# Kernel tuning notes

Measured on AMD Instinct MI355X. Metric: run time of the kernel, lower is better.

## Reference

```python
import jax, jax.numpy as jnp
import numpy as np

EPS = 1e-5

def layernorm(x, g, b):
    mu = x.mean(-1, keepdims=True)
    var = ((x - mu) ** 2).mean(-1, keepdims=True)
    return (x - mu) / jnp.sqrt(var + EPS) * g + b

def segment_softmax(logits, seg, num_seg):
    # logits: [E, H, Q]; softmax over edges sharing the same target segment
    m = jax.ops.segment_max(logits, seg, num_segments=num_seg)
    ex = jnp.exp(logits - m[seg])
    s = jax.ops.segment_sum(ex, seg, num_segments=num_seg)
    return ex / s[seg]

def mha(x, Kw, Qw, Vw, tgt, src, n_tgt):
    # x: [N_src, C]; Kw/Vw: [H, C, D]; Qw: [H, Q, D]
    xK = jnp.einsum('nc,hcd->hnd', x, Kw)
    alpha = jnp.einsum('hqd,hnd->hqn', Qw, xK)            # [H, Q, N_src]
    a_e = alpha.transpose(2, 0, 1)[src]                   # [E, H, Q] per-edge logits
    w = segment_softmax(a_e, tgt, n_tgt)                  # sparse softmax over sources per target
    xV = jnp.einsum('nc,hcd->hnd', x, Vw)                 # [H, N_src, D]
    msg = w[..., None] * xV.transpose(1, 0, 2)[src][:, :, None, :]  # [E, H, Q, D]
    return jax.ops.segment_sum(msg, tgt, num_segments=n_tgt)        # [n_tgt, H, Q, D]

def block(x, tgt, src, n_tgt, Kw, Qw, Vw, g0, b0, W1, W2, g1, b1):
    Qn = Qw.shape[1]
    h = mha(x, Kw, Qw, Vw, tgt, src, n_tgt) + Qw          # [n_tgt, H, Q, D]
    h = h.transpose(0, 2, 1, 3).reshape(n_tgt, Qn, -1)    # [n_tgt, Q, hidden]
    h = layernorm(h, g0, b0)
    m = jax.nn.relu(jax.nn.relu(h @ W1) @ W2)             # MLP(Linear,ReLU,Linear) + outer ReLU
    h = layernorm(h + m, g1, b1)
    return h.sum(axis=1)                                  # [n_tgt, hidden]

def setup_inputs() -> dict:
    key = jax.random.key(0)
    ks = jax.random.split(key, 12)
    N, M, E, C, H, Q, D = 50000, 20000, 1000000, 128, 4, 1, 32
    HID = H * D
    s = 0.1
    inp = {
        'x_0': jax.random.normal(ks[0], (N, C), jnp.float32),
        'node_idx': jax.random.randint(ks[1], (E,), 0, N),
        'hedge_idx': jax.random.randint(ks[2], (E,), 0, M),
        'n_nodes': N,
        'n_hedges': M,
        'v2e_K': jax.random.normal(ks[3], (H, C, D), jnp.float32) * s,
        'v2e_Q': jax.random.normal(ks[4], (H, Q, D), jnp.float32) * s,
        'v2e_V': jax.random.normal(ks[5], (H, C, D), jnp.float32) * s,
        'v2e_ln0_g': jnp.ones((HID,), jnp.float32),
        'v2e_ln0_b': jnp.zeros((HID,), jnp.float32),
        'v2e_W1': jax.random.normal(ks[6], (HID, HID), jnp.float32) * s,
        'v2e_W2': jax.random.normal(ks[7], (HID, HID), jnp.float32) * s,
        'v2e_ln1_g': jnp.ones((HID,), jnp.float32),
        'v2e_ln1_b': jnp.zeros((HID,), jnp.float32),
        'e2v_K': jax.random.normal(ks[8], (H, HID, D), jnp.float32) * s,
        'e2v_Q': jax.random.normal(ks[9], (H, Q, D), jnp.float32) * s,
        'e2v_V': jax.random.normal(ks[10], (H, HID, D), jnp.float32) * s,
        'e2v_ln0_g': jnp.ones((HID,), jnp.float32),
        'e2v_ln0_b': jnp.zeros((HID,), jnp.float32),
        'e2v_W1': jax.random.normal(ks[11], (HID, HID), jnp.float32) * s,
        'e2v_W2': jax.random.normal(jax.random.fold_in(key, 99), (HID, HID), jnp.float32) * s,
        'e2v_ln1_g': jnp.ones((HID,), jnp.float32),
        'e2v_ln1_b': jnp.zeros((HID,), jnp.float32),
    }
    return inp

def reference(x_0, node_idx, hedge_idx, n_nodes, n_hedges,
              v2e_K, v2e_Q, v2e_V, v2e_ln0_g, v2e_ln0_b, v2e_W1, v2e_W2, v2e_ln1_g, v2e_ln1_b,
              e2v_K, e2v_Q, e2v_V, e2v_ln0_g, e2v_ln0_b, e2v_W1, e2v_W2, e2v_ln1_g, e2v_ln1_b):
    # vertex -> hyperedge: neighborhood = incidence^T, targets = hyperedges, sources = nodes
    x_1 = jax.nn.relu(block(x_0, hedge_idx, node_idx, n_hedges,
                            v2e_K, v2e_Q, v2e_V, v2e_ln0_g, v2e_ln0_b,
                            v2e_W1, v2e_W2, v2e_ln1_g, v2e_ln1_b))
    # hyperedge -> vertex: neighborhood = incidence, targets = nodes, sources = hyperedges
    x_0_out = jax.nn.relu(block(x_1, node_idx, hedge_idx, n_nodes,
                                e2v_K, e2v_Q, e2v_V, e2v_ln0_g, e2v_ln0_b,
                                e2v_W1, e2v_W2, e2v_ln1_g, e2v_ln1_b))
    return x_0_out, x_1
```

## Files before the change

kernel.cpp:

```cpp
#include <hip/hip_runtime.h>
#include <math.h>

typedef __attribute__((ext_vector_type(8))) short bf16x8;
typedef __attribute__((ext_vector_type(4))) float f32x4;

#define CSR_P 256

__device__ __forceinline__ unsigned short f2bf(float f){
  union { float f; unsigned int u; } c; c.f = f;
  unsigned int u = c.u;
  u += 0x7fff + ((u >> 16) & 1);
  return (unsigned short)(u >> 16);
}

__device__ __forceinline__ float wsum64(float v){
  #pragma unroll
  for (int off = 32; off > 0; off >>= 1) v += __shfl_xor(v, off, 64);
  return v;
}

__global__ __launch_bounds__(256) void prep2_kernel(
    const float* __restrict__ K0, const float* __restrict__ Q0, const float* __restrict__ V0,
    const float* __restrict__ W10, const float* __restrict__ W20,
    const float* __restrict__ K1, const float* __restrict__ Q1, const float* __restrict__ V1,
    const float* __restrict__ W11, const float* __restrict__ W21,
    float* __restrict__ kq0, unsigned short* __restrict__ btV0,
    unsigned short* __restrict__ btW10, unsigned short* __restrict__ btW20,
    float* __restrict__ kq1, unsigned short* __restrict__ btV1,
    unsigned short* __restrict__ btW11, unsigned short* __restrict__ btW21){
  const float *K, *Q, *V, *W1, *W2; float* kq;
  unsigned short *btV, *btW1, *btW2;
  if (blockIdx.y == 0){ K=K0; Q=Q0; V=V0; W1=W10; W2=W20; kq=kq0; btV=btV0; btW1=btW10; btW2=btW20; }
  else                { K=K1; Q=Q1; V=V1; W1=W11; W2=W21; kq=kq1; btV=btV1; btW1=btW11; btW2=btW21; }
  int i = blockIdx.x * 256 + threadIdx.x;
  if (i < 512){
    int h = i >> 7, c = i & 127;
    const float* Kp = K + (size_t)h * 4096 + (size_t)c * 32;
    const float* Qp = Q + h * 32;
    float s = 0.f;
    #pragma unroll
    for (int d = 0; d < 32; ++d) s += Kp[d] * Qp[d];
    kq[i] = s;
    return;
  }
  int j = i - 512;
  if (j < 16384){
    int n = j >> 7, k = j & 127;
    int h = n >> 5, d = n & 31;
    btV[j] = f2bf(V[(size_t)h * 4096 + (size_t)k * 32 + d]);
    return;
  }
  j -= 16384;
  if (j < 16384){
    int n = j >> 7, k = j & 127;
    btW1[j] = f2bf(W1[(size_t)k * 128 + n]);
    return;
  }
  j -= 16384;
  if (j < 16384){
    int n = j >> 7, k = j & 127;
    btW2[j] = f2bf(W2[(size_t)k * 128 + n]);
  }
}

__global__ __launch_bounds__(256) void logits_kernel(const float* __restrict__ x,
                                                     const float* __restrict__ kq,
                                                     float* __restrict__ expl,
                                                     unsigned short* __restrict__ xb,
                                                     unsigned short* __restrict__ xv,
                                                     int R){
  int row = (blockIdx.x << 2) + (threadIdx.x >> 6);
  if (row > R) return;
  int lane = threadIdx.x & 63;
  if (row == R){
    if (lane < 4) expl[4 * (size_t)R + lane] = 0.f;
    ((unsigned*)xv)[((size_t)R << 6) + lane] = 0u;
    return;
  }
  float x1 = x[128 * (size_t)row + lane];
  float x2 = x[128 * (size_t)row + lane + 64];
  xb[128 * (size_t)row + lane]      = f2bf(x1);
  xb[128 * (size_t)row + lane + 64] = f2bf(x2);
  float p0 = x1 * kq[lane]       + x2 * kq[lane + 64];
  float p1 = x1 * kq[128 + lane] + x2 * kq[192 + lane];
  float p2 = x1 * kq[256 + lane] + x2 * kq[320 + lane];
  float p3 = x1 * kq[384 + lane] + x2 * kq[448 + lane];
  p0 = wsum64(p0); p1 = wsum64(p1); p2 = wsum64(p2); p3 = wsum64(p3);
  if (lane == 0)
    *(float4*)(expl + 4 * (size_t)row) =
        make_float4(__expf(p0), __expf(p1), __expf(p2), __expf(p3));
}

__global__ __launch_bounds__(256) void hist2_kernel(const int* __restrict__ tgt0, int NB0,
                                                    const int* __restrict__ tgt1, int NB1,
                                                    int E,
                                                    int* __restrict__ counts0,
                                                    int* __restrict__ counts1){
  const int* tgt; int NB; int* counts;
  if (blockIdx.y == 0){ tgt = tgt0; NB = NB0; counts = counts0; }
  else                { tgt = tgt1; NB = NB1; counts = counts1; }
  __shared__ int hist[256];
  for (int i = threadIdx.x; i < NB; i += 256) hist[i] = 0;
  __syncthreads();
  int chunk = (E + CSR_P - 1) / CSR_P;
  int b0 = blockIdx.x * chunk, b1 = min(b0 + chunk, E);
  for (int e = b0 + threadIdx.x; e < b1; e += 256)
    atomicAdd(&hist[tgt[e] >> 8], 1);
  __syncthreads();
  for (int i = threadIdx.x; i < NB; i += 256)
    counts[i * CSR_P + blockIdx.x] = hist[i];
}

__global__ __launch_bounds__(256) void bscan_kernel(const int* __restrict__ counts0, int NB0,
                                                    const int* __restrict__ counts1,
                                                    int* __restrict__ blkoff0, int* __restrict__ blkoff1,
                                                    int* __restrict__ btot0, int* __restrict__ btot1){
  int i = blockIdx.x;
  const int* counts; int* blkoff; int* btot; int b;
  if (i < NB0){ counts = counts0; blkoff = blkoff0; btot = btot0; b = i; }
  else        { counts = counts1; blkoff = blkoff1; btot = btot1; b = i - NB0; }
  __shared__ int wtmp[5];
  int tid = threadIdx.x, lane = tid & 63, wv = tid >> 6;
  int c = counts[b * CSR_P + tid];
  int s = c;
  #pragma unroll
  for (int off = 1; off < 64; off <<= 1){
    int t = __shfl_up(s, off, 64);
    if (lane >= off) s += t;
  }
  if (lane == 63) wtmp[wv] = s;
  __syncthreads();
  if (tid == 0){
    int a0 = wtmp[0], a1 = wtmp[1], a2 = wtmp[2], a3 = wtmp[3];
    wtmp[0] = 0; wtmp[1] = a0; wtmp[2] = a0 + a1; wtmp[3] = a0 + a1 + a2;
    wtmp[4] = a0 + a1 + a2 + a3;
  }
  __syncthreads();
  blkoff[b * CSR_P + tid] = s - c + wtmp[wv];
  if (tid == 0) btot[b] = wtmp[4];
}

__global__ __launch_bounds__(64) void base_scan_kernel(const int* __restrict__ btot0, int NB0,
                                                       int* __restrict__ base0,
                                                       const int* __restrict__ btot1, int NB1,
                                                       int* __restrict__ base1){
  int lane = threadIdx.x;
  for (int pass = 0; pass < 2; ++pass){
    const int* bt = pass ? btot1 : btot0;
    int* bs       = pass ? base1 : base0;
    int NB        = pass ? NB1   : NB0;
    int carry = 0;
    for (int s0 = 0; s0 < NB; s0 += 64){
      int i = s0 + lane;
      int v = (i < NB) ? bt[i] : 0;
      int s = v;
      #pragma unroll
      for (int off = 1; off < 64; off <<= 1){
        int t = __shfl_up(s, off, 64);
        if (lane >= off) s += t;
      }
      if (i < NB) bs[i] = carry + s - v;
      carry += __shfl(s, 63, 64);
    }
  }
}

__global__ __launch_bounds__(256) void scatter2_kernel(
    const int* __restrict__ tgt0, const int* __restrict__ src0, int NB0,
    const int* __restrict__ base0, const int* __restrict__ blkoff0, int2* __restrict__ pairs0,
    const int* __restrict__ tgt1, const int* __restrict__ src1, int NB1,
    const int* __restrict__ base1, const int* __restrict__ blkoff1, int2* __restrict__ pairs1,
    int E){
  const int *tgt, *src, *bbase, *boff; int NB; int2* pairs;
  if (blockIdx.y == 0){ tgt=tgt0; src=src0; bbase=base0; boff=blkoff0; NB=NB0; pairs=pairs0; }
  else                { tgt=tgt1; src=src1; bbase=base1; boff=blkoff1; NB=NB1; pairs=pairs1; }
  __shared__ int cur[256];
  for (int i = threadIdx.x; i < NB; i += 256)
    cur[i] = bbase[i] + boff[i * CSR_P + blockIdx.x];
  __syncthreads();
  int chunk = (E + CSR_P - 1) / CSR_P;
  int b0 = blockIdx.x * chunk, b1 = min(b0 + chunk, E);
  for (int e = b0 + threadIdx.x; e < b1; e += 256){
    int t = tgt[e];
    int pos = atomicAdd(&cur[t >> 8], 1);
    pairs[pos] = make_int2(src[e], t);
  }
}

__global__ __launch_bounds__(1024) void build2_kernel(
    const int* __restrict__ base0, const int* __restrict__ btot0, int NB0,
    const int2* __restrict__ pairs0, int n0, int d0,
    int* __restrict__ rp0, int* __restrict__ kc0, int* __restrict__ col0,
    const int* __restrict__ base1, const int* __restrict__ btot1, int NB1,
    const int2* __restrict__ pairs1, int n1, int d1,
    int* __restrict__ rp1, int* __restrict__ kc1, int* __restrict__ col1){
  int b = blockIdx.x;
  const int *bbase, *bt; const int2* pairs; int n_tgt, dummy;
  int *rowptr, *kcnt, *col;
  if (blockIdx.y == 0){
    if (b >= NB0) return;
    bbase=base0; bt=btot0; pairs=pairs0; n_tgt=n0; dummy=d0; rowptr=rp0; kcnt=kc0; col=col0;
  } else {
    if (b >= NB1) return;
    bbase=base1; bt=btot1; pairs=pairs1; n_tgt=n1; dummy=d1; rowptr=rp1; kcnt=kc1; col=col1;
  }
  __shared__ int hist[256];
  __shared__ int excl[256];
  __shared__ int cur[256];
  int tid = threadIdx.x;
  int start = bbase[b];
  int end   = start + bt[b];
  int col_base = ((start + 3) & ~3) + (b << 10);
  for (int i = tid; i < 256; i += 1024) hist[i] = 0;
  __syncthreads();
  for (int e = start + tid; e < end; e += 1024)
    atomicAdd(&hist[pairs[e].y & 255], 1);
  __syncthreads();
  if (tid < 64){
    int lane = tid;
    int p0 = (hist[4 * lane]     + 3) & ~3;
    int p1 = (hist[4 * lane + 1] + 3) & ~3;
    int p2 = (hist[4 * lane + 2] + 3) & ~3;
    int p3 = (hist[4 * lane + 3] + 3) & ~3;
    int tsum = p0 + p1 + p2 + p3;
    int s = tsum;
    #pragma unroll
    for (int off = 1; off < 64; off <<= 1){
      int t = __shfl_up(s, off, 64);
      if (lane >= off) s += t;
    }
    int e0 = s - tsum;
    excl[4 * lane]     = e0;
    excl[4 * lane + 1] = e0 + p0;
    excl[4 * lane + 2] = e0 + p0 + p1;
    excl[4 * lane + 3] = e0 + p0 + p1 + p2;
  }
  __syncthreads();
  int t0 = b << 8;
  int valid = min(256, n_tgt - t0);
  for (int i = tid; i < valid; i += 1024){
    rowptr[t0 + i] = col_base + excl[i];
    kcnt[t0 + i]   = (hist[i] + 3) & ~3;
  }
  for (int i = tid; i < 256; i += 1024) cur[i] = excl[i];
  __syncthreads();
  for (int e = start + tid; e < end; e += 1024){
    int2 p = pairs[e];
    int pos = atomicAdd(&cur[p.y & 255], 1);
    col[col_base + pos] = p.x;
  }
  __syncthreads();
  for (int i = tid; i < valid; i += 1024){
    int hc = hist[i], pc = (hc + 3) & ~3;
    int base = col_base + excl[i];
    for (int j = hc; j < pc; ++j) col[base + j] = dummy;
  }
}

__global__ __launch_bounds__(256) void agg_kernel(const int* __restrict__ rowptr,
                                                  const int* __restrict__ kcnt,
                                                  const int* __restrict__ col,
                                                  const float* __restrict__ expl,
                                                  const unsigned short* __restrict__ xV,
                                                  const float* __restrict__ qvec,
                                                  const float* __restrict__ g0,
                                                  const float* __restrict__ b0,
                                                  float* __restrict__ h_out,
                                                  unsigned short* __restrict__ hb_out,
                                                  int n_tgt){
  int wid = (blockIdx.x << 2) + (threadIdx.x >> 6);
  if (wid >= n_tgt) return;
  int lane = threadIdx.x & 63;
  unsigned head = (unsigned)(lane >> 4);
  int beg = rowptr[wid];
  int k   = kcnt[wid];

  const unsigned* xv32 = (const unsigned*)xV;
  float accx = 0.f, accy = 0.f, sumw = 0.f;
  #pragma unroll 2
  for (int e = 0; e < k; e += 4){
    int4 cc = *(const int4*)(col + beg + e);
    #pragma unroll
    for (int q = 0; q < 4; ++q){
      int se = (q == 0) ? cc.x : (q == 1) ? cc.y : (q == 2) ? cc.z : cc.w;
      float a = expl[((unsigned)se << 2) + head];
      unsigned v = xv32[((unsigned)se << 6) + lane];
      union { unsigned u; float f; } lo, hi;
      lo.u = v << 16;
      hi.u = v & 0xffff0000u;
      sumw += a;
      accx += a * lo.f;
      accy += a * hi.f;
    }
  }
  float inv = (sumw > 0.f) ? 1.f / sumw : 0.f;
  accx *= inv; accy *= inv;

  float2 q2 = *(const float2*)(qvec + 2 * lane);
  accx += q2.x; accy += q2.y;

  float mean = wsum64(accx + accy) * (1.f / 128.f);
  float dx = accx - mean, dy = accy - mean;
  float var = wsum64(dx * dx + dy * dy) * (1.f / 128.f);
  float rstd = rsqrtf(var + 1e-5f);
  float2 g = *(const float2*)(g0 + 2 * lane);
  float2 b = *(const float2*)(b0 + 2 * lane);
  float ox = dx * rstd * g.x + b.x;
  float oy = dy * rstd * g.y + b.y;
  *(float2*)(h_out + 128 * (size_t)wid + 2 * lane) = make_float2(ox, oy);
  unsigned int pk = ((unsigned int)f2bf(oy) << 16) | (unsigned int)f2bf(ox);
  *(unsigned int*)(hb_out + 128 * (size_t)wid + 2 * lane) = pk;
}

__global__ __launch_bounds__(256) void gemm_xv(const unsigned short* __restrict__ A,
                                               const unsigned short* __restrict__ Bt,
                                               unsigned short* __restrict__ C, int R){
  __shared__ unsigned short As[64 * 136];
  __shared__ unsigned short Bs[128 * 136];
  int tid = threadIdx.x;
  int row0 = blockIdx.x * 64;

  #pragma unroll
  for (int i = 0; i < 16; ++i){
    int f = tid + i * 256;
    int n = f >> 5, c4 = f & 31;
    *(ushort4*)&Bs[n * 136 + c4 * 4] = *(const ushort4*)(Bt + n * 128 + c4 * 4);
  }
  #pragma unroll
  for (int i = 0; i < 8; ++i){
    int f = tid + i * 256;
    int r = f >> 5, c4 = f & 31;
    ushort4 v = make_ushort4(0, 0, 0, 0);
    if (row0 + r < R) v = *(const ushort4*)(A + (size_t)(row0 + r) * 128 + c4 * 4);
    *(ushort4*)&As[r * 136 + c4 * 4] = v;
  }
  __syncthreads();

  int lane = tid & 63, wv = tid >> 6;
  int m = lane & 15, quad = lane >> 4;
  f32x4 acc[8];
  #pragma unroll
  for (int j = 0; j < 8; ++j) acc[j] = (f32x4){0.f, 0.f, 0.f, 0.f};

  #pragma unroll
  for (int q = 0; q < 4; ++q){
    bf16x8 a = *(const bf16x8*)&As[(wv * 16 + m) * 136 + q * 32 + quad * 8];
    #pragma unroll
    for (int j = 0; j < 8; ++j){
      bf16x8 b = *(const bf16x8*)&Bs[(j * 16 + m) * 136 + q * 32 + quad * 8];
      acc[j] = __builtin_amdgcn_mfma_f32_16x16x32_bf16(a, b, acc[j], 0, 0, 0);
    }
  }

  #pragma unroll
  for (int j = 0; j < 8; ++j){
    int colc = j * 16 + m;
    #pragma unroll
    for (int r = 0; r < 4; ++r){
      int gr = row0 + wv * 16 + quad * 4 + r;
      if (gr < R) C[(size_t)gr * 128 + colc] = f2bf(acc[j][r]);
    }
  }
}

__global__ __launch_bounds__(256) void mfma_mlp_ln(const unsigned short* __restrict__ A,
                                                   const unsigned short* __restrict__ Bt1,
                                                   const unsigned short* __restrict__ Bt2,
                                                   const float* __restrict__ h,
                                                   const float* __restrict__ g,
                                                   const float* __restrict__ b,
                                                   float* __restrict__ outp, int R){
  __shared__ unsigned short As[64 * 136];
  __shared__ unsigned short Bs[128 * 136];
  int tid = threadIdx.x;
  int row0 = blockIdx.x * 64;

  #pragma unroll
  for (int i = 0; i < 16; ++i){
    int f = tid + i * 256;
    int n = f >> 5, c4 = f & 31;
    *(ushort4*)&Bs[n * 136 + c4 * 4] = *(const ushort4*)(Bt1 + n * 128 + c4 * 4);
  }
  #pragma unroll
  for (int i = 0; i < 8; ++i){
    int f = tid + i * 256;
    int r = f >> 5, c4 = f & 31;
    ushort4 v = make_ushort4(0, 0, 0, 0);
    if (row0 + r < R) v = *(const ushort4*)(A + (size_t)(row0 + r) * 128 + c4 * 4);
    *(ushort4*)&As[r * 136 + c4 * 4] = v;
  }
  __syncthreads();

  int lane = tid & 63, wv = tid >> 6;
  int m = lane & 15, quad = lane >> 4;
  f32x4 acc[8];
  #pragma unroll
  for (int j = 0; j < 8; ++j) acc[j] = (f32x4){0.f, 0.f, 0.f, 0.f};

  #pragma unroll
  for (int q = 0; q < 4; ++q){
    bf16x8 a = *(const bf16x8*)&As[(wv * 16 + m) * 136 + q * 32 + quad * 8];
    #pragma unroll
    for (int j = 0; j < 8; ++j){
      bf16x8 b8 = *(const bf16x8*)&Bs[(j * 16 + m) * 136 + q * 32 + quad * 8];
      acc[j] = __builtin_amdgcn_mfma_f32_16x16x32_bf16(a, b8, acc[j], 0, 0, 0);
    }
  }
  __syncthreads();

  #pragma unroll
  for (int j = 0; j < 8; ++j){
    #pragma unroll
    for (int r = 0; r < 4; ++r)
      As[(wv * 16 + quad * 4 + r) * 136 + j * 16 + m] = f2bf(fmaxf(acc[j][r], 0.f));
  }
  #pragma unroll
  for (int i = 0; i < 16; ++i){
    int f = tid + i * 256;
    int n = f >> 5, c4 = f & 31;
    *(ushort4*)&Bs[n * 136 + c4 * 4] = *(const ushort4*)(Bt2 + n * 128 + c4 * 4);
  }
  __syncthreads();

  #pragma unroll
  for (int j = 0; j < 8; ++j) acc[j] = (f32x4){0.f, 0.f, 0.f, 0.f};
  #pragma unroll
  for (int q = 0; q < 4; ++q){
    bf16x8 a = *(const bf16x8*)&As[(wv * 16 + m) * 136 + q * 32 + quad * 8];
    #pragma unroll
    for (int j = 0; j < 8; ++j){
      bf16x8 b8 = *(const bf16x8*)&Bs[(j * 16 + m) * 136 + q * 32 + quad * 8];
      acc[j] = __builtin_amdgcn_mfma_f32_16x16x32_bf16(a, b8, acc[j], 0, 0, 0);
    }
  }

  float gv[8], bv[8];
  #pragma unroll
  for (int j = 0; j < 8; ++j){ gv[j] = g[j * 16 + m]; bv[j] = b[j * 16 + m]; }

  #pragma unroll
  for (int r = 0; r < 4; ++r){
    int gr = row0 + wv * 16 + quad * 4 + r;
    if (gr >= R) continue;
    float v[8];
    float s = 0.f;
    #pragma unroll
    for (int j = 0; j < 8; ++j){
      float mm = fmaxf(acc[j][r], 0.f);
      v[j] = h[(size_t)gr * 128 + j * 16 + m] + mm;
      s += v[j];
    }
    s += __shfl_xor(s, 1, 64); s += __shfl_xor(s, 2, 64);
    s += __shfl_xor(s, 4, 64); s += __shfl_xor(s, 8, 64);
    float mean = s * (1.f / 128.f);
    float s2 = 0.f;
    #pragma unroll
    for (int j = 0; j < 8; ++j){ v[j] -= mean; s2 += v[j] * v[j]; }
    s2 += __shfl_xor(s2, 1, 64); s2 += __shfl_xor(s2, 2, 64);
    s2 += __shfl_xor(s2, 4, 64); s2 += __shfl_xor(s2, 8, 64);
    float rstd = rsqrtf(s2 * (1.f / 128.f) + 1e-5f);
    #pragma unroll
    for (int j = 0; j < 8; ++j)
      outp[(size_t)gr * 128 + j * 16 + m] = fmaxf(v[j] * rstd * gv[j] + bv[j], 0.f);
  }
}

struct Ws {
  float *kq0, *kq1, *expl, *h;
  unsigned short *btV0, *btW10, *btW20, *btV1, *btW11, *btW21, *xv, *hb;
};

static void run_stage(const float* x_f32, int R_src,
                      const int* rowptr, const int* kcnt, const int* col, int n_tgt,
                      const float* kq, const unsigned short* btV,
                      const unsigned short* btW1, const unsigned short* btW2,
                      const float* Qw, const float* g0, const float* b0,
                      const float* g1, const float* b1,
                      float* out, const Ws& ws, hipStream_t stream)
{
  logits_kernel<<<(R_src + 1 + 3) / 4, 256, 0, stream>>>(x_f32, kq, ws.expl, ws.hb, ws.xv, R_src);
  gemm_xv<<<(R_src + 63) / 64, 256, 0, stream>>>(ws.hb, btV, ws.xv, R_src);
  agg_kernel<<<(n_tgt + 3) / 4, 256, 0, stream>>>(rowptr, kcnt, col, ws.expl, ws.xv,
                                                  Qw, g0, b0, ws.h, ws.hb, n_tgt);
  mfma_mlp_ln<<<(n_tgt + 63) / 64, 256, 0, stream>>>(ws.hb, btW1, btW2, ws.h, g1, b1, out, n_tgt);
}

extern "C" void kernel_launch(void* const* d_in, const int* in_sizes, int n_in,
                              void* d_out, int out_size, void* d_ws, size_t ws_size,
                              hipStream_t stream)
{
  const float* x0        = (const float*)d_in[0];
  const int*   node_idx  = (const int*)d_in[1];
  const int*   hedge_idx = (const int*)d_in[2];
  const float* v2e_K = (const float*)d_in[5];
  const float* v2e_Q = (const float*)d_in[6];
  const float* v2e_V = (const float*)d_in[7];
  const float* v2e_g0 = (const float*)d_in[8];
  const float* v2e_b0 = (const float*)d_in[9];
  const float* v2e_W1 = (const float*)d_in[10];
  const float* v2e_W2 = (const float*)d_in[11];
  const float* v2e_g1 = (const float*)d_in[12];
  const float* v2e_b1 = (const float*)d_in[13];
  const float* e2v_K = (const float*)d_in[14];
  const float* e2v_Q = (const float*)d_in[15];
  const float* e2v_V = (const float*)d_in[16];
  const float* e2v_g0 = (const float*)d_in[17];
  const float* e2v_b0 = (const float*)d_in[18];
  const float* e2v_W1 = (const float*)d_in[19];
  const float* e2v_W2 = (const float*)d_in[20];
  const float* e2v_g1 = (const float*)d_in[21];
  const float* e2v_b1 = (const float*)d_in[22];

  int N = in_sizes[0] / 128;
  int E = in_sizes[1];
  int M = out_size / 128 - N;

  float* out_x0 = (float*)d_out;
  float* out_x1 = (float*)d_out + (size_t)N * 128;

  size_t off = 0;
  char* base = (char*)d_ws;
  auto alloc = [&](size_t bytes) -> void* {
    void* p = base + off;
    off += (bytes + 255) & ~(size_t)255;
    return p;
  };
  int NB0 = (M + 255) >> 8;
  int NB1 = (N + 255) >> 8;
  int NBmax = NB1 > NB0 ? NB1 : NB0;
  size_t colcap = (size_t)E + 1024 * (size_t)NBmax + 64;

  Ws ws;
  ws.kq0   = (float*)alloc(512 * 4);
  ws.kq1   = (float*)alloc(512 * 4);
  ws.btV0  = (unsigned short*)alloc(16384 * 2);
  ws.btW10 = (unsigned short*)alloc(16384 * 2);
  ws.btW20 = (unsigned short*)alloc(16384 * 2);
  ws.btV1  = (unsigned short*)alloc(16384 * 2);
  ws.btW11 = (unsigned short*)alloc(16384 * 2);
  ws.btW21 = (unsigned short*)alloc(16384 * 2);
  ws.expl  = (float*)alloc(((size_t)N + 1) * 4 * 4);
  size_t uoff = off;
  ws.xv    = (unsigned short*)alloc(((size_t)N + 1) * 128 * 2);
  ws.hb    = (unsigned short*)alloc((size_t)N * 128 * 2);
  ws.h     = (float*)alloc((size_t)N * 128 * 4);
  int2* pairs0 = (int2*)(base + uoff);
  int2* pairs1 = pairs0 + E;
  int* counts0 = (int*)(pairs1 + E);
  int* counts1 = counts0 + 256 * CSR_P;
  int* blkoff0 = counts1 + 256 * CSR_P;
  int* blkoff1 = blkoff0 + 256 * CSR_P;
  int* btot0   = blkoff1 + 256 * CSR_P;
  int* btot1   = btot0 + 256;
  int* base0   = btot1 + 256;
  int* base1   = base0 + 256;
  int* rowptr0 = (int*)alloc((size_t)M * 4);
  int* kcnt0   = (int*)alloc((size_t)M * 4);
  int* col0    = (int*)alloc(colcap * 4);
  int* rowptr1 = (int*)alloc((size_t)N * 4);
  int* kcnt1   = (int*)alloc((size_t)N * 4);
  int* col1    = (int*)alloc(colcap * 4);
  (void)ws_size; (void)n_in;

  prep2_kernel<<<dim3(194, 2), 256, 0, stream>>>(
      v2e_K, v2e_Q, v2e_V, v2e_W1, v2e_W2,
      e2v_K, e2v_Q, e2v_V, e2v_W1, e2v_W2,
      ws.kq0, ws.btV0, ws.btW10, ws.btW20,
      ws.kq1, ws.btV1, ws.btW11, ws.btW21);

  hist2_kernel<<<dim3(CSR_P, 2), 256, 0, stream>>>(hedge_idx, NB0, node_idx, NB1, E,
                                                   counts0, counts1);
  bscan_kernel<<<NB0 + NB1, 256, 0, stream>>>(counts0, NB0, counts1,
                                              blkoff0, blkoff1, btot0, btot1);
  base_scan_kernel<<<1, 64, 0, stream>>>(btot0, NB0, base0, btot1, NB1, base1);
  scatter2_kernel<<<dim3(CSR_P, 2), 256, 0, stream>>>(
      hedge_idx, node_idx, NB0, base0, blkoff0, pairs0,
      node_idx, hedge_idx, NB1, base1, blkoff1, pairs1, E);
  build2_kernel<<<dim3(NBmax, 2), 1024, 0, stream>>>(
      base0, btot0, NB0, pairs0, M, N, rowptr0, kcnt0, col0,
      base1, btot1, NB1, pairs1, N, M, rowptr1, kcnt1, col1);

  run_stage(x0, N, rowptr0, kcnt0, col0, M,
            ws.kq0, ws.btV0, ws.btW10, ws.btW20,
            v2e_Q, v2e_g0, v2e_b0, v2e_g1, v2e_b1,
            out_x1, ws, stream);

  run_stage(out_x1, M, rowptr1, kcnt1, col1, N,
            ws.kq1, ws.btV1, ws.btW11, ws.btW21,
            e2v_Q, e2v_g0, e2v_b0, e2v_g1, e2v_b1,
            out_x0, ws, stream);
}
```

Measured before the change: 316.9 us.

## Fuse logits into xV GEMM via split-bf16 kq columns, pack CSR pairs, drop fp32 h

```diff
diff --git a/kernel.cpp b/kernel.cpp
--- a/kernel.cpp
+++ b/kernel.cpp
@@ -12,6 +12,10 @@
   u += 0x7fff + ((u >> 16) & 1);
   return (unsigned short)(u >> 16);
 }
+__device__ __forceinline__ float bf2f(unsigned short h){
+  union { unsigned int u; float f; } c; c.u = ((unsigned int)h) << 16;
+  return c.f;
+}
 
 __device__ __forceinline__ float wsum64(float v){
   #pragma unroll
@@ -24,14 +28,14 @@
     const float* __restrict__ W10, const float* __restrict__ W20,
     const float* __restrict__ K1, const float* __restrict__ Q1, const float* __restrict__ V1,
     const float* __restrict__ W11, const float* __restrict__ W21,
-    float* __restrict__ kq0, unsigned short* __restrict__ btV0,
+    unsigned short* __restrict__ btV0, unsigned short* __restrict__ btkq0,
     unsigned short* __restrict__ btW10, unsigned short* __restrict__ btW20,
-    float* __restrict__ kq1, unsigned short* __restrict__ btV1,
+    unsigned short* __restrict__ btV1, unsigned short* __restrict__ btkq1,
     unsigned short* __restrict__ btW11, unsigned short* __restrict__ btW21){
-  const float *K, *Q, *V, *W1, *W2; float* kq;
-  unsigned short *btV, *btW1, *btW2;
-  if (blockIdx.y == 0){ K=K0; Q=Q0; V=V0; W1=W10; W2=W20; kq=kq0; btV=btV0; btW1=btW10; btW2=btW20; }
-  else                { K=K1; Q=Q1; V=V1; W1=W11; W2=W21; kq=kq1; btV=btV1; btW1=btW11; btW2=btW21; }
+  const float *K, *Q, *V, *W1, *W2;
+  unsigned short *btV, *btkq, *btW1, *btW2;
+  if (blockIdx.y == 0){ K=K0; Q=Q0; V=V0; W1=W10; W2=W20; btV=btV0; btkq=btkq0; btW1=btW10; btW2=btW20; }
+  else                { K=K1; Q=Q1; V=V1; W1=W11; W2=W21; btV=btV1; btkq=btkq1; btW1=btW11; btW2=btW21; }
   int i = blockIdx.x * 256 + threadIdx.x;
   if (i < 512){
     int h = i >> 7, c = i & 127;
@@ -40,7 +44,9 @@
     float s = 0.f;
     #pragma unroll
     for (int d = 0; d < 32; ++d) s += Kp[d] * Qp[d];
-    kq[i] = s;
+    unsigned short hi = f2bf(s);
+    btkq[h * 128 + c]       = hi;
+    btkq[(4 + h) * 128 + c] = f2bf(s - bf2f(hi));
     return;
   }
   int j = i - 512;
@@ -61,34 +67,6 @@
     int n = j >> 7, k = j & 127;
     btW2[j] = f2bf(W2[(size_t)k * 128 + n]);
   }
-}
-
-__global__ __launch_bounds__(256) void logits_kernel(const float* __restrict__ x,
-                                                     const float* __restrict__ kq,
-                                                     float* __restrict__ expl,
-                                                     unsigned short* __restrict__ xb,
-                                                     unsigned short* __restrict__ xv,
-                                                     int R){
-  int row = (blockIdx.x << 2) + (threadIdx.x >> 6);
-  if (row > R) return;
-  int lane = threadIdx.x & 63;
-  if (row == R){
-    if (lane < 4) expl[4 * (size_t)R + lane] = 0.f;
-    ((unsigned*)xv)[((size_t)R << 6) + lane] = 0u;
-    return;
-  }
-  float x1 = x[128 * (size_t)row + lane];
-  float x2 = x[128 * (size_t)row + lane + 64];
-  xb[128 * (size_t)row + lane]      = f2bf(x1);
-  xb[128 * (size_t)row + lane + 64] = f2bf(x2);
-  float p0 = x1 * kq[lane]       + x2 * kq[lane + 64];
-  float p1 = x1 * kq[128 + lane] + x2 * kq[192 + lane];
-  float p2 = x1 * kq[256 + lane] + x2 * kq[320 + lane];
-  float p3 = x1 * kq[384 + lane] + x2 * kq[448 + lane];
-  p0 = wsum64(p0); p1 = wsum64(p1); p2 = wsum64(p2); p3 = wsum64(p3);
-  if (lane == 0)
-    *(float4*)(expl + 4 * (size_t)row) =
-        make_float4(__expf(p0), __expf(p1), __expf(p2), __expf(p3));
 }
 
 __global__ __launch_bounds__(256) void hist2_kernel(const int* __restrict__ tgt0, int NB0,
@@ -167,11 +145,11 @@
 
 __global__ __launch_bounds__(256) void scatter2_kernel(
     const int* __restrict__ tgt0, const int* __restrict__ src0, int NB0,
-    const int* __restrict__ base0, const int* __restrict__ blkoff0, int2* __restrict__ pairs0,
+    const int* __restrict__ base0, const int* __restrict__ blkoff0, int* __restrict__ pairs0,
     const int* __restrict__ tgt1, const int* __restrict__ src1, int NB1,
-    const int* __restrict__ base1, const int* __restrict__ blkoff1, int2* __restrict__ pairs1,
+    const int* __restrict__ base1, const int* __restrict__ blkoff1, int* __restrict__ pairs1,
     int E){
-  const int *tgt, *src, *bbase, *boff; int NB; int2* pairs;
+  const int *tgt, *src, *bbase, *boff; int NB; int* pairs;
   if (blockIdx.y == 0){ tgt=tgt0; src=src0; bbase=base0; boff=blkoff0; NB=NB0; pairs=pairs0; }
   else                { tgt=tgt1; src=src1; bbase=base1; boff=blkoff1; NB=NB1; pairs=pairs1; }
   __shared__ int cur[256];
@@ -183,19 +161,19 @@
   for (int e = b0 + threadIdx.x; e < b1; e += 256){
     int t = tgt[e];
     int pos = atomicAdd(&cur[t >> 8], 1);
-    pairs[pos] = make_int2(src[e], t);
+    pairs[pos] = ((t & 255) << 24) | src[e];
   }
 }
 
 __global__ __launch_bounds__(1024) void build2_kernel(
     const int* __restrict__ base0, const int* __restrict__ btot0, int NB0,
-    const int2* __restrict__ pairs0, int n0, int d0,
+    const int* __restrict__ pairs0, int n0, int d0,
     int* __restrict__ rp0, int* __restrict__ kc0, int* __restrict__ col0,
     const int* __restrict__ base1, const int* __restrict__ btot1, int NB1,
-    const int2* __restrict__ pairs1, int n1, int d1,
+    const int* __restrict__ pairs1, int n1, int d1,
     int* __restrict__ rp1, int* __restrict__ kc1, int* __restrict__ col1){
   int b = blockIdx.x;
-  const int *bbase, *bt; const int2* pairs; int n_tgt, dummy;
+  const int *bbase, *bt; const int* pairs; int n_tgt, dummy;
   int *rowptr, *kcnt, *col;
   if (blockIdx.y == 0){
     if (b >= NB0) return;
@@ -214,7 +192,7 @@
   for (int i = tid; i < 256; i += 1024) hist[i] = 0;
   __syncthreads();
   for (int e = start + tid; e < end; e += 1024)
-    atomicAdd(&hist[pairs[e].y & 255], 1);
+    atomicAdd(&hist[(pairs[e] >> 24) & 255], 1);
   __syncthreads();
   if (tid < 64){
     int lane = tid;
@@ -245,15 +223,81 @@
   for (int i = tid; i < 256; i += 1024) cur[i] = excl[i];
   __syncthreads();
   for (int e = start + tid; e < end; e += 1024){
-    int2 p = pairs[e];
-    int pos = atomicAdd(&cur[p.y & 255], 1);
-    col[col_base + pos] = p.x;
+    int p = pairs[e];
+    int pos = atomicAdd(&cur[(p >> 24) & 255], 1);
+    col[col_base + pos] = p & 0xFFFFFF;
   }
   __syncthreads();
   for (int i = tid; i < valid; i += 1024){
     int hc = hist[i], pc = (hc + 3) & ~3;
     int base = col_base + excl[i];
     for (int j = hc; j < pc; ++j) col[base + j] = dummy;
+  }
+}
+
+__global__ __launch_bounds__(256) void gemm_xvl(const float* __restrict__ x,
+                                                const unsigned short* __restrict__ btV,
+                                                const unsigned short* __restrict__ btkq,
+                                                unsigned short* __restrict__ xv,
+                                                float* __restrict__ expl, int R){
+  __shared__ unsigned short As[64 * 136];
+  __shared__ unsigned short Bs[144 * 136];
+  int tid = threadIdx.x;
+  int row0 = blockIdx.x * 64;
+
+  #pragma unroll
+  for (int i = 0; i < 16; ++i){
+    int f = tid + i * 256;
+    int n = f >> 5, c4 = f & 31;
+    *(ushort4*)&Bs[n * 136 + c4 * 4] = *(const ushort4*)(btV + n * 128 + c4 * 4);
+  }
+  {
+    int n = tid >> 5, c4 = tid & 31;
+    *(ushort4*)&Bs[(128 + n) * 136 + c4 * 4] = *(const ushort4*)(btkq + n * 128 + c4 * 4);
+  }
+  #pragma unroll
+  for (int i = 0; i < 8; ++i){
+    int f = tid + i * 256;
+    int r = f >> 5, c4 = f & 31;
+    float4 v = make_float4(0.f, 0.f, 0.f, 0.f);
+    if (row0 + r < R) v = *(const float4*)(x + (size_t)(row0 + r) * 128 + c4 * 4);
+    ushort4 h;
+    h.x = f2bf(v.x); h.y = f2bf(v.y); h.z = f2bf(v.z); h.w = f2bf(v.w);
+    *(ushort4*)&As[r * 136 + c4 * 4] = h;
+  }
+  __syncthreads();
+
+  int lane = tid & 63, wv = tid >> 6;
+  int m = lane & 15, quad = lane >> 4;
+  f32x4 acc[9];
+  #pragma unroll
+  for (int j = 0; j < 9; ++j) acc[j] = (f32x4){0.f, 0.f, 0.f, 0.f};
+
+  #pragma unroll
+  for (int q = 0; q < 4; ++q){
+    bf16x8 a = *(const bf16x8*)&As[(wv * 16 + m) * 136 + q * 32 + quad * 8];
+    #pragma unroll
+    for (int j = 0; j < 9; ++j){
+      bf16x8 b = *(const bf16x8*)&Bs[(j * 16 + m) * 136 + q * 32 + quad * 8];
+      acc[j] = __builtin_amdgcn_mfma_f32_16x16x32_bf16(a, b, acc[j], 0, 0, 0);
+    }
+  }
+
+  #pragma unroll
+  for (int j = 0; j < 8; ++j){
+    int colc = j * 16 + m;
+    #pragma unroll
+    for (int r = 0; r < 4; ++r){
+      int gr = row0 + wv * 16 + quad * 4 + r;
+      if (gr <= R) xv[(size_t)gr * 128 + colc] = f2bf(acc[j][r]);
+    }
+  }
+  #pragma unroll
+  for (int r = 0; r < 4; ++r){
+    int gr = row0 + wv * 16 + quad * 4 + r;
+    float lg = acc[8][r] + __shfl_xor(acc[8][r], 4, 64);
+    if (m < 4 && gr <= R)
+      expl[(size_t)gr * 4 + m] = (gr == R) ? 0.f : __expf(lg);
   }
 }
 
@@ -265,7 +309,6 @@
                                                   const float* __restrict__ qvec,
                                                   const float* __restrict__ g0,
                                                   const float* __restrict__ b0,
-                                                  float* __restrict__ h_out,
                                                   unsigned short* __restrict__ hb_out,
                                                   int n_tgt){
   int wid = (blockIdx.x << 2) + (threadIdx.x >> 6);
@@ -307,66 +350,13 @@
   float2 b = *(const float2*)(b0 + 2 * lane);
   float ox = dx * rstd * g.x + b.x;
   float oy = dy * rstd * g.y + b.y;
-  *(float2*)(h_out + 128 * (size_t)wid + 2 * lane) = make_float2(ox, oy);
   unsigned int pk = ((unsigned int)f2bf(oy) << 16) | (unsigned int)f2bf(ox);
   *(unsigned int*)(hb_out + 128 * (size_t)wid + 2 * lane) = pk;
-}
-
-__global__ __launch_bounds__(256) void gemm_xv(const unsigned short* __restrict__ A,
-                                               const unsigned short* __restrict__ Bt,
-                                               unsigned short* __restrict__ C, int R){
-  __shared__ unsigned short As[64 * 136];
-  __shared__ unsigned short Bs[128 * 136];
-  int tid = threadIdx.x;
-  int row0 = blockIdx.x * 64;
-
-  #pragma unroll
-  for (int i = 0; i < 16; ++i){
-    int f = tid + i * 256;
-    int n = f >> 5, c4 = f & 31;
-    *(ushort4*)&Bs[n * 136 + c4 * 4] = *(const ushort4*)(Bt + n * 128 + c4 * 4);
-  }
-  #pragma unroll
-  for (int i = 0; i < 8; ++i){
-    int f = tid + i * 256;
-    int r = f >> 5, c4 = f & 31;
-    ushort4 v = make_ushort4(0, 0, 0, 0);
-    if (row0 + r < R) v = *(const ushort4*)(A + (size_t)(row0 + r) * 128 + c4 * 4);
-    *(ushort4*)&As[r * 136 + c4 * 4] = v;
-  }
-  __syncthreads();
-
-  int lane = tid & 63, wv = tid >> 6;
-  int m = lane & 15, quad = lane >> 4;
-  f32x4 acc[8];
-  #pragma unroll
-  for (int j = 0; j < 8; ++j) acc[j] = (f32x4){0.f, 0.f, 0.f, 0.f};
-
-  #pragma unroll
-  for (int q = 0; q < 4; ++q){
-    bf16x8 a = *(const bf16x8*)&As[(wv * 16 + m) * 136 + q * 32 + quad * 8];
-    #pragma unroll
-    for (int j = 0; j < 8; ++j){
-      bf16x8 b = *(const bf16x8*)&Bs[(j * 16 + m) * 136 + q * 32 + quad * 8];
-      acc[j] = __builtin_amdgcn_mfma_f32_16x16x32_bf16(a, b, acc[j], 0, 0, 0);
-    }
-  }
-
-  #pragma unroll
-  for (int j = 0; j < 8; ++j){
-    int colc = j * 16 + m;
-    #pragma unroll
-    for (int r = 0; r < 4; ++r){
-      int gr = row0 + wv * 16 + quad * 4 + r;
-      if (gr < R) C[(size_t)gr * 128 + colc] = f2bf(acc[j][r]);
-    }
-  }
 }
 
 __global__ __launch_bounds__(256) void mfma_mlp_ln(const unsigned short* __restrict__ A,
                                                    const unsigned short* __restrict__ Bt1,
                                                    const unsigned short* __restrict__ Bt2,
-                                                   const float* __restrict__ h,
                                                    const float* __restrict__ g,
                                                    const float* __restrict__ b,
                                                    float* __restrict__ outp, int R){
@@ -406,6 +396,13 @@
       acc[j] = __builtin_amdgcn_mfma_f32_16x16x32_bf16(a, b8, acc[j], 0, 0, 0);
     }
   }
+
+  float res[4][8];
+  #pragma unroll
+  for (int r = 0; r < 4; ++r)
+    #pragma unroll
+    for (int j = 0; j < 8; ++j)
+      res[r][j] = bf2f(As[(wv * 16 + quad * 4 + r) * 136 + j * 16 + m]);
   __syncthreads();
 
   #pragma unroll
@@ -447,7 +444,7 @@
     #pragma unroll
     for (int j = 0; j < 8; ++j){
       float mm = fmaxf(acc[j][r], 0.f);
-      v[j] = h[(size_t)gr * 128 + j * 16 + m] + mm;
+      v[j] = res[r][j] + mm;
       s += v[j];
     }
     s += __shfl_xor(s, 1, 64); s += __shfl_xor(s, 2, 64);
@@ -466,23 +463,22 @@
 }
 
 struct Ws {
-  float *kq0, *kq1, *expl, *h;
-  unsigned short *btV0, *btW10, *btW20, *btV1, *btW11, *btW21, *xv, *hb;
+  float *expl;
+  unsigned short *btV0, *btkq0, *btW10, *btW20, *btV1, *btkq1, *btW11, *btW21, *xv, *hb;
 };
 
 static void run_stage(const float* x_f32, int R_src,
                       const int* rowptr, const int* kcnt, const int* col, int n_tgt,
-                      const float* kq, const unsigned short* btV,
+                      const unsigned short* btV, const unsigned short* btkq,
                       const unsigned short* btW1, const unsigned short* btW2,
                       const float* Qw, const float* g0, const float* b0,
                       const float* g1, const float* b1,
                       float* out, const Ws& ws, hipStream_t stream)
 {
-  logits_kernel<<<(R_src + 1 + 3) / 4, 256, 0, stream>>>(x_f32, kq, ws.expl, ws.hb, ws.xv, R_src);
-  gemm_xv<<<(R_src + 63) / 64, 256, 0, stream>>>(ws.hb, btV, ws.xv, R_src);
+  gemm_xvl<<<(R_src + 1 + 63) / 64, 256, 0, stream>>>(x_f32, btV, btkq, ws.xv, ws.expl, R_src);
   agg_kernel<<<(n_tgt + 3) / 4, 256, 0, stream>>>(rowptr, kcnt, col, ws.expl, ws.xv,
-                                                  Qw, g0, b0, ws.h, ws.hb, n_tgt);
-  mfma_mlp_ln<<<(n_tgt + 63) / 64, 256, 0, stream>>>(ws.hb, btW1, btW2, ws.h, g1, b1, out, n_tgt);
+                                                  Qw, g0, b0, ws.hb, n_tgt);
+  mfma_mlp_ln<<<(n_tgt + 63) / 64, 256, 0, stream>>>(ws.hb, btW1, btW2, g1, b1, out, n_tgt);
 }
 
 extern "C" void kernel_launch(void* const* d_in, const int* in_sizes, int n_in,
@@ -531,22 +527,21 @@
   size_t colcap = (size_t)E + 1024 * (size_t)NBmax + 64;
 
   Ws ws;
-  ws.kq0   = (float*)alloc(512 * 4);
-  ws.kq1   = (float*)alloc(512 * 4);
   ws.btV0  = (unsigned short*)alloc(16384 * 2);
+  ws.btkq0 = (unsigned short*)alloc(1024 * 2);
   ws.btW10 = (unsigned short*)alloc(16384 * 2);
   ws.btW20 = (unsigned short*)alloc(16384 * 2);
   ws.btV1  = (unsigned short*)alloc(16384 * 2);
+  ws.btkq1 = (unsigned short*)alloc(1024 * 2);
   ws.btW11 = (unsigned short*)alloc(16384 * 2);
   ws.btW21 = (unsigned short*)alloc(16384 * 2);
   ws.expl  = (float*)alloc(((size_t)N + 1) * 4 * 4);
   size_t uoff = off;
   ws.xv    = (unsigned short*)alloc(((size_t)N + 1) * 128 * 2);
   ws.hb    = (unsigned short*)alloc((size_t)N * 128 * 2);
-  ws.h     = (float*)alloc((size_t)N * 128 * 4);
-  int2* pairs0 = (int2*)(base + uoff);
-  int2* pairs1 = pairs0 + E;
-  int* counts0 = (int*)(pairs1 + E);
+  int* pairs0  = (int*)(base + uoff);
+  int* pairs1  = pairs0 + E;
+  int* counts0 = pairs1 + E;
   int* counts1 = counts0 + 256 * CSR_P;
   int* blkoff0 = counts1 + 256 * CSR_P;
   int* blkoff1 = blkoff0 + 256 * CSR_P;
@@ -565,8 +560,8 @@
   prep2_kernel<<<dim3(194, 2), 256, 0, stream>>>(
       v2e_K, v2e_Q, v2e_V, v2e_W1, v2e_W2,
       e2v_K, e2v_Q, e2v_V, e2v_W1, e2v_W2,
-      ws.kq0, ws.btV0, ws.btW10, ws.btW20,
-      ws.kq1, ws.btV1, ws.btW11, ws.btW21);
+      ws.btV0, ws.btkq0, ws.btW10, ws.btW20,
+      ws.btV1, ws.btkq1, ws.btW11, ws.btW21);
 
   hist2_kernel<<<dim3(CSR_P, 2), 256, 0, stream>>>(hedge_idx, NB0, node_idx, NB1, E,
                                                    counts0, counts1);
@@ -581,12 +576,12 @@
       base1, btot1, NB1, pairs1, N, M, rowptr1, kcnt1, col1);
 
   run_stage(x0, N, rowptr0, kcnt0, col0, M,
-            ws.kq0, ws.btV0, ws.btW10, ws.btW20,
+            ws.btV0, ws.btkq0, ws.btW10, ws.btW20,
             v2e_Q, v2e_g0, v2e_b0, v2e_g1, v2e_b1,
             out_x1, ws, stream);
 
   run_stage(out_x1, M, rowptr1, kcnt1, col1, N,
-            ws.kq1, ws.btV1, ws.btW11, ws.btW21,
+            ws.btV1, ws.btkq1, ws.btW11, ws.btW21,
             e2v_Q, e2v_g0, e2v_b0, e2v_g1, e2v_b1,
             out_x0, ws, stream);
 }
```

After: 296.4 us. 6.5% less time.
